# Kernel optimization log

Measured on AMD Instinct MI355X. Metric: run time of the kernel, lower is better.

The kernel has to match this reference:

```python
import jax, jax.numpy as jnp
import numpy as np

B, L, C, W, NH, FS = 8, 8, 64, 32, 128, 5
PAD = FS // 2
LN_EPS = 1e-5


def _conv(x, w, b, pad):
    y = jax.lax.conv_general_dilated(x, w, (1, 1), [(pad, pad), (pad, pad)],
                                     dimension_numbers=('NCHW', 'OIHW', 'NCHW'))
    return y + b[None, :, None, None]


def _stem(x, w1, b1, lnw, lnb, w2, b2):
    # conv(fs) -> LayerNorm over [C,W,W] -> ReLU -> conv(1x1)
    y = _conv(x, w1, b1, PAD)
    mu = jnp.mean(y, axis=(1, 2, 3), keepdims=True)
    var = jnp.var(y, axis=(1, 2, 3), keepdims=True)
    y = (y - mu) * jax.lax.rsqrt(var + LN_EPS) * lnw[None] + lnb[None]
    return _conv(jax.nn.relu(y), w2, b2, 0)


def setup_inputs() -> dict:
    key = jax.random.key(0)
    ks = jax.random.split(key, 8)
    f = lambda k, shp: jax.random.normal(k, shp, jnp.float32) * 0.02
    return {
        'in_query': jax.random.normal(ks[0], (B, C, W, W), jnp.float32),
        'in_keys': jax.random.normal(ks[1], (B, L, C, W, W), jnp.float32),
        'in_values': jax.random.normal(ks[2], (B, L, C, W, W), jnp.float32),
        's_w1': f(ks[3], (C, C, FS, FS)), 's_b1': jnp.zeros((C,), jnp.float32),
        's_lnw': jnp.ones((C, W, W), jnp.float32), 's_lnb': jnp.zeros((C, W, W), jnp.float32),
        's_w2': f(ks[4], (NH, C, 1, 1)), 's_b2': jnp.zeros((NH,), jnp.float32),
        'c_w1': f(ks[5], (C, C, FS, FS)), 'c_b1': jnp.zeros((C,), jnp.float32),
        'c_lnw': jnp.ones((C, W, W), jnp.float32), 'c_lnb': jnp.zeros((C, W, W), jnp.float32),
        'c_w2': f(ks[6], (NH, C, 1, 1)), 'c_b2': jnp.zeros((NH,), jnp.float32),
    }


def reference(in_query, in_keys, in_values,
              s_w1, s_b1, s_lnw, s_lnb, s_w2, s_b2,
              c_w1, c_b1, c_lnw, c_lnb, c_w2, c_b2):
    b, c, w, h = in_query.shape
    l = in_keys.shape[1]
    # ---- spatial attention: tokens = pixels, features = channels ----
    qf = in_query.reshape(b, c, w * h).transpose(0, 2, 1)            # [B, WH, C]
    kf = in_keys.transpose(0, 1, 3, 4, 2).reshape(b, l * w * h, c)   # [B, LWH, C]
    vf = in_values.transpose(0, 1, 3, 4, 2).reshape(b, l * w * h, c)
    a_sp = jax.nn.softmax(jnp.einsum('bnc,bmc->bnm', qf, kf), axis=-1)  # [B, WH, LWH]
    sp = jnp.einsum('bnm,bmc->bnc', a_sp, vf).reshape(b, w, h, c).transpose(0, 3, 1, 2)
    # ---- channel attention: tokens = channels, features = pixels ----
    qc = in_query.reshape(b, c, w * h)                               # [B, C, WH]
    kc = in_keys.reshape(b, l * c, h * w)                            # [B, LC, WH]
    vc = in_values.reshape(b, l * c, h * w)
    a_ch = jax.nn.softmax(jnp.einsum('bcn,bmn->bcm', qc, kc), axis=-1)  # [B, C, LC]
    ch = jnp.einsum('bcm,bmn->bcn', a_ch, vc).reshape(b, c, w, h)
    # ---- conv-LN-ReLU-conv stems on residual-added branches ----
    s_attn = _stem(sp + in_query, s_w1, s_b1, s_lnw, s_lnb, s_w2, s_b2)
    c_attn = _stem(ch + in_query, c_w1, c_b1, c_lnw, c_lnb, c_w2, c_b2)
    return (s_attn, c_attn)
```

## Files before the change

### kernel.cpp

```cpp
#include <hip/hip_runtime.h>


#define LOG2E 1.44269504088896340736f

typedef __attribute__((ext_vector_type(8))) short short8;
typedef __attribute__((ext_vector_type(4))) float f4;

#define MFMA16(a, b, c) __builtin_amdgcn_mfma_f32_16x16x32_bf16(a, b, c, 0, 0, 0)

#define GLOAD_LDS16(gp, lp) __builtin_amdgcn_global_load_lds( \
    (const __attribute__((address_space(1))) void*)(gp), \
    (__attribute__((address_space(3))) void*)(lp), 16, 0, 0)

__device__ __forceinline__ unsigned short f2bf(float f) {
  union { float f; unsigned u; } v; v.f = f;
  unsigned r = v.u + 0x7FFFu + ((v.u >> 16) & 1u);
  return (unsigned short)(r >> 16);
}
__device__ __forceinline__ unsigned short f2bf_rz(float f) {
  union { float f; unsigned u; } v; v.f = f;
  return (unsigned short)(v.u >> 16);
}
__device__ __forceinline__ float bf2f(unsigned short h) {
  union { unsigned u; float f; } v; v.u = ((unsigned)h) << 16;
  return v.f;
}
__device__ __forceinline__ float exp2fast(float x) {
#if __has_builtin(__builtin_amdgcn_exp2f)
  return __builtin_amdgcn_exp2f(x);
#else
  return exp2f(x);
#endif
}

#define O_STATS 0ul
#define O_W1T   256ul
#define O_W2B   409856ul
#define O_LNW   442624ul
#define O_LNB   704768ul
#define O_QT    966912ul
#define O_KSP   2015488ul
#define O_VT    10404096ul
#define O_NUM   18792704ul
#define O_DEN   35569920ul
#define O_SP    36094208ul
#define O_PCH   40288512ul
#define O_XS    40812800ul
#define O_XC    41861376ul
#define O_YT    42909952ul

__global__ __launch_bounds__(256) void k1_prep(
    const float* __restrict__ q, const float* __restrict__ keys,
    const float* __restrict__ values,
    const float* __restrict__ sw1, const float* __restrict__ slnw,
    const float* __restrict__ slnb, const float* __restrict__ sw2,
    const float* __restrict__ cw1, const float* __restrict__ clnw,
    const float* __restrict__ clnb, const float* __restrict__ cw2,
    char* __restrict__ ws)
{
  __shared__ __align__(16) unsigned char SM1[49152];
  const int t = threadIdx.x;

  if (blockIdx.x < 128) {
    float* Sp = (float*)(ws + O_SP);
    const int bid = blockIdx.x;
    if (bid == 0 && t < 64) ((float*)(ws + O_STATS))[t] = 0.f;
    const int b = bid >> 4, colT = (bid >> 2) & 3, kt = bid & 3;
    const int w = t >> 6, lane = t & 63;
    const int low4 = lane & 15, quad = lane >> 4;
    const int dl = lane >> 1, dh = lane & 1;
    const int k00 = kt * 256;

    f4 acc[4][2];
#pragma unroll
    for (int m = 0; m < 4; ++m)
#pragma unroll
      for (int n = 0; n < 2; ++n) acc[m][n] = (f4){0.f, 0.f, 0.f, 0.f};

    auto stageAll = [&](int bo, int k0) {
#pragma unroll
      for (int gi = 0; gi < 4; ++gi) {
        const int g = w + gi * 4;
        const int n = g >> 1, sub = g & 1;
        const int l = sub * 32 + dl;
        const float* gp = keys + (size_t)(b * 512 + colT * 128 + n * 16 + (l & 15)) * 1024
                          + k0 + (l >> 4) * 8 + dh * 4;
        GLOAD_LDS16(gp, SM1 + bo + (size_t)(n * 128 + sub * 64) * 16);
      }
#pragma unroll
      for (int gi = 0; gi < 2; ++gi) {
        const int g = w + gi * 4;
        const int m = g >> 1, sub = g & 1;
        const int l = sub * 32 + dl;
        const float* gp = q + (size_t)(b * 64 + m * 16 + (l & 15)) * 1024
                          + k0 + (l >> 4) * 8 + dh * 4;
        GLOAD_LDS16(gp, SM1 + bo + 16384 + (size_t)(m * 128 + sub * 64) * 16);
      }
    };

    stageAll(0, k00);
    for (int it = 0; it < 8; ++it) {
      const int bo = (it & 1) * 24576;
      const char* cb = (const char*)SM1 + bo;
      __syncthreads();
      if (it < 7) stageAll(bo ^ 24576, k00 + (it + 1) * 32);

      short8 ah[4], al[4];
#pragma unroll
      for (int m = 0; m < 4; ++m) {
        const float* fp = (const float*)(cb + 16384 + (size_t)(m * 128 + lane * 2) * 16);
        float4 u0 = ((const float4*)fp)[0];
        float4 u1 = ((const float4*)fp)[1];
        float vv[8] = {u0.x, u0.y, u0.z, u0.w, u1.x, u1.y, u1.z, u1.w};
#pragma unroll
        for (int j = 0; j < 8; ++j) {
          float sv = vv[j] * LOG2E;
          unsigned short hi = f2bf(sv);
          ah[m][j] = (short)hi;
          al[m][j] = (short)f2bf(sv - bf2f(hi));
        }
      }
#pragma unroll
      for (int n2 = 0; n2 < 2; ++n2) {
        const int n = w * 2 + n2;
        const float* fp = (const float*)(cb + (size_t)(n * 128 + lane * 2) * 16);
        float4 u0 = ((const float4*)fp)[0];
        float4 u1 = ((const float4*)fp)[1];
        float vv[8] = {u0.x, u0.y, u0.z, u0.w, u1.x, u1.y, u1.z, u1.w};
        short8 bh, bl;
#pragma unroll
        for (int j = 0; j < 8; ++j) {
          unsigned short hi = f2bf(vv[j]);
          bh[j] = (short)hi;
          bl[j] = (short)f2bf(vv[j] - bf2f(hi));
        }
#pragma unroll
        for (int m = 0; m < 4; ++m) {
          acc[m][n2] = MFMA16(ah[m], bh, acc[m][n2]);
          acc[m][n2] = MFMA16(al[m], bh, acc[m][n2]);
          acc[m][n2] = MFMA16(ah[m], bl, acc[m][n2]);
        }
      }
    }

#pragma unroll
    for (int m = 0; m < 4; ++m)
#pragma unroll
      for (int n2 = 0; n2 < 2; ++n2)
#pragma unroll
        for (int r = 0; r < 4; ++r) {
          const int row = m * 16 + quad * 4 + r;
          const int col = colT * 128 + (w * 2 + n2) * 16 + low4;
          Sp[(((size_t)kt * 8 + b) * 64 + row) * 512 + col] = acc[m][n2][r];
        }
    return;
  }

  float (*T)[65] = (float(*)[65])SM1;
  const int job = blockIdx.x - 128;

  if (job < 2240) {
    int kind, mat = 0, sel = 0;
    if (job < 1024)      { kind = 0; mat = job >> 4; }
    else if (job < 2048) { kind = 1; mat = (job - 1024) >> 4; }
    else if (job < 2176) { kind = 2; mat = (job - 2048) >> 4; }
    else                 { kind = 3; sel = (job - 2176) >> 4; }
    const int pt = job & 15, p0 = pt * 64;
    const float* src =
        kind == 0 ? keys : kind == 1 ? values : kind == 2 ? q
        : (sel == 0 ? slnw : sel == 1 ? slnb : sel == 2 ? clnw : clnb);
    src += (size_t)mat * 65536;

    const int r0 = t >> 4, c4 = (t & 15) * 4;
    if (kind == 1) {
      unsigned short* VTp = (unsigned short*)(ws + O_VT);
      const int b = mat >> 3, l = mat & 7;
#pragma unroll
      for (int pass = 0; pass < 4; ++pass) {
        const int r = pass * 16 + r0;
        float4 v = *(const float4*)(src + (size_t)r * 1024 + p0 + c4);
        ushort4 o;
        o.x = f2bf(v.x); o.y = f2bf(v.y); o.z = f2bf(v.z); o.w = f2bf(v.w);
        *(ushort4*)(VTp + ((size_t)b * 64 + r) * 8192 + l * 1024 + p0 + c4) = o;
      }
      return;
    }
#pragma unroll
    for (int pass = 0; pass < 4; ++pass) {
      const int r = pass * 16 + r0;
      float4 v = *(const float4*)(src + (size_t)r * 1024 + p0 + c4);
      T[r][c4] = v.x; T[r][c4 + 1] = v.y; T[r][c4 + 2] = v.z; T[r][c4 + 3] = v.w;
    }
    __syncthreads();
#pragma unroll
    for (int pass = 0; pass < 2; ++pass) {
      const int p = pass * 32 + (t >> 3), cs = (t & 7) * 8;
      short8 o;
      if (kind == 0) {
#pragma unroll
        for (int j = 0; j < 8; ++j) o[j] = (short)f2bf(T[cs + j][p] * LOG2E);
        const int b = mat >> 3, l = mat & 7;
        *(short8*)((unsigned short*)(ws + O_KSP) +
                   ((size_t)b * 8192 + l * 1024 + p0 + p) * 64 + cs) = o;
      } else if (kind == 2) {
#pragma unroll
        for (int j = 0; j < 8; ++j) o[j] = (short)f2bf(T[cs + j][p]);
        *(short8*)((unsigned short*)(ws + O_QT) +
                   ((size_t)mat * 1024 + p0 + p) * 64 + cs) = o;
      } else {
#pragma unroll
        for (int j = 0; j < 8; ++j) o[j] = (short)f2bf(T[cs + j][p]);
        unsigned long off = (sel & 1) ? O_LNB : O_LNW;
        *(short8*)((unsigned short*)(ws + off) +
                   ((size_t)(sel >> 1) * 1024 + p0 + p) * 64 + cs) = o;
      }
    }
    return;
  }

  {
    unsigned i = (job - 2240) * 256u + t;
    if (i < 204800u) {
      unsigned ci = i & 63u, co = (i >> 6) & 63u, tt = i >> 12;
      unsigned off = tt % 25u, st = tt / 25u;
      const float* w = st ? cw1 : sw1;
      ((unsigned short*)(ws + O_W1T))[i] = f2bf(w[(co * 64u + ci) * 25u + off]);
      return;
    }
    i -= 204800u;
    if (i < 16384u) {
      unsigned c = i & 63u, nh = (i >> 6) & 127u, st = i >> 13;
      const float* w = st ? cw2 : sw2;
      ((unsigned short*)(ws + O_W2B))[i] = f2bf(w[nh * 64u + c]);
    }
  }
}

__global__ __launch_bounds__(256) void k2_spat(char* __restrict__ ws)
{
  __shared__ __align__(16) unsigned char SM[65536];

  unsigned short (*Kt)[4096] = (unsigned short(*)[4096])(SM);
  unsigned short (*Vt)[4096] = (unsigned short(*)[4096])(SM + 16384);
  unsigned short (*Pl)[4096] = (unsigned short(*)[4096])(SM + 32768);

  const unsigned short* QT = (const unsigned short*)(ws + O_QT);
  const unsigned short* KSP = (const unsigned short*)(ws + O_KSP);
  const unsigned short* VTg = (const unsigned short*)(ws + O_VT);
  unsigned short* NUM = (unsigned short*)(ws + O_NUM);
  float* DEN = (float*)(ws + O_DEN);

  const int b = blockIdx.x >> 6;
  const int qt = (blockIdx.x >> 4) & 3;
  const int s = blockIdx.x & 15;
  const int t = threadIdx.x;
  const int w = t >> 6, lane = t & 63;
  const int low4 = lane & 15, quad = lane >> 4;

  const unsigned short* KSPb = KSP + (size_t)b * 8192 * 64;
  const unsigned short* VTb = VTg + (size_t)b * 64 * 8192;
  const int qbase = qt * 256 + w * 64;
  const int kvbase = s * 512;

  int cn[2], cks[2], cqd[2], cl4[2];
#pragma unroll
  for (int pass = 0; pass < 2; ++pass) {
    const int c = pass * 256 + t;
    cn[pass] = c >> 7; cks[pass] = (c >> 6) & 1;
    cqd[pass] = (c >> 4) & 3; cl4[pass] = c & 15;
  }

  short8 qa[4][2];
#pragma unroll
  for (int mi = 0; mi < 4; ++mi)
#pragma unroll
    for (int ks = 0; ks < 2; ++ks)
      qa[mi][ks] = *(const short8*)(QT +
          ((size_t)(b * 1024 + qbase + mi * 16 + low4)) * 64 + ks * 32 + quad * 8);

  short8 vones;
#pragma unroll
  for (int j = 0; j < 8; ++j) vones[j] = (short)0x3F80;

  f4 accO[4][4], accD[4];
#pragma unroll
  for (int m = 0; m < 4; ++m) {
    accD[m] = (f4){0.f, 0.f, 0.f, 0.f};
#pragma unroll
    for (int n = 0; n < 4; ++n) accO[m][n] = (f4){0.f, 0.f, 0.f, 0.f};
  }

#pragma unroll
  for (int pass = 0; pass < 2; ++pass) {
    GLOAD_LDS16(KSPb + ((size_t)(kvbase + cn[pass] * 16 + cl4[pass])) * 64 +
                    cks[pass] * 32 + cqd[pass] * 8,
                &Kt[0][(pass * 256 + w * 64) * 8]);
    GLOAD_LDS16(VTb + ((size_t)(cn[pass] * 16 + cl4[pass])) * 8192 + kvbase +
                    cks[pass] * 32 + cqd[pass] * 8,
                &Vt[0][(pass * 256 + w * 64) * 8]);
  }

  const int pswz = ((low4 >> 2) & 3) << 1;
  for (int it = 0; it < 8; ++it) {
    const int d = it & 1;
    __syncthreads();
    if (it < 7) {
      const int kv1 = kvbase + (it + 1) * 64;
#pragma unroll
      for (int pass = 0; pass < 2; ++pass) {
        GLOAD_LDS16(KSPb + ((size_t)(kv1 + cn[pass] * 16 + cl4[pass])) * 64 +
                        cks[pass] * 32 + cqd[pass] * 8,
                    &Kt[d ^ 1][(pass * 256 + w * 64) * 8]);
        GLOAD_LDS16(VTb + ((size_t)(cn[pass] * 16 + cl4[pass])) * 8192 + kv1 +
                        cks[pass] * 32 + cqd[pass] * 8,
                    &Vt[d ^ 1][(pass * 256 + w * 64) * 8]);
      }
    }
#pragma unroll
    for (int n = 0; n < 4; ++n) {
      f4 sS[4];
#pragma unroll
      for (int mi = 0; mi < 4; ++mi) sS[mi] = (f4){0.f, 0.f, 0.f, 0.f};
#pragma unroll
      for (int ks = 0; ks < 2; ++ks) {
        short8 kb = *(const short8*)&Kt[d][((n * 2 + ks) * 64 + lane) * 8];
#pragma unroll
        for (int mi = 0; mi < 4; ++mi) sS[mi] = MFMA16(qa[mi][ks], kb, sS[mi]);
      }
      const int cpr = (((n * 2 + (low4 >> 3)) ^ (quad << 1)) << 3) + (low4 & 7);
#pragma unroll
      for (int mi = 0; mi < 4; ++mi) {
        unsigned short* pw = &Pl[w][(mi * 16 + quad * 4) * 64 + cpr];
#pragma unroll
        for (int r = 0; r < 4; ++r)
          pw[r * 64] = f2bf_rz(exp2fast(sS[mi][r]));
      }
    }
#pragma unroll
    for (int ks = 0; ks < 2; ++ks) {
      short8 vb[4];
#pragma unroll
      for (int n2 = 0; n2 < 4; ++n2)
        vb[n2] = *(const short8*)&Vt[d][((n2 * 2 + ks) * 64 + lane) * 8];
      const int cr = (((ks * 4 + quad) ^ pswz) << 3);
#pragma unroll
      for (int m = 0; m < 4; ++m) {
        short8 pa = *(const short8*)&Pl[w][(m * 16 + low4) * 64 + cr];
        accD[m] = MFMA16(pa, vones, accD[m]);
#pragma unroll
        for (int n2 = 0; n2 < 4; ++n2) accO[m][n2] = MFMA16(pa, vb[n2], accO[m][n2]);
      }
    }
  }

#pragma unroll
  for (int m = 0; m < 4; ++m)
#pragma unroll
    for (int r = 0; r < 4; ++r) {
      const int row = qbase + m * 16 + quad * 4 + r;
      const size_t base = ((size_t)(b * 1024 + row) * 16 + s);
#pragma unroll
      for (int n2 = 0; n2 < 4; ++n2)
        NUM[base * 64 + n2 * 16 + low4] = f2bf(accO[m][n2][r]);
      if (low4 == 0) DEN[base] = accD[m][r];
    }
}

__global__ __launch_bounds__(256) void k3_fin_soft(char* __restrict__ ws)
{
  if (blockIdx.x < 512) {
    const unsigned short* NUM = (const unsigned short*)(ws + O_NUM);
    const float* DEN = (const float*)(ws + O_DEN);
    const unsigned short* QT = (const unsigned short*)(ws + O_QT);
    unsigned short* Xs = (unsigned short*)(ws + O_XS);

    const unsigned i = blockIdx.x * 256u + threadIdx.x;
    const int c0 = (i & 15) * 4;
    const unsigned row = i >> 4;

    float dtot = 0.f;
#pragma unroll
    for (int sq = 0; sq < 4; ++sq) {
      float4 dv = *(const float4*)(DEN + (size_t)row * 16 + sq * 4);
      dtot += dv.x + dv.y + dv.z + dv.w;
    }
    float n4[4] = {0.f, 0.f, 0.f, 0.f};
#pragma unroll
    for (int s = 0; s < 16; ++s) {
      ushort4 pv = *(const ushort4*)(NUM + ((size_t)row * 16 + s) * 64 + c0);
      n4[0] += bf2f(pv.x); n4[1] += bf2f(pv.y);
      n4[2] += bf2f(pv.z); n4[3] += bf2f(pv.w);
    }
    const float rd = 1.0f / dtot;
    size_t ob = (size_t)row * 64 + c0;
    ushort4 qv = *(const ushort4*)(QT + ob);
    ushort4 o4;
    o4.x = f2bf(n4[0] * rd + bf2f(qv.x));
    o4.y = f2bf(n4[1] * rd + bf2f(qv.y));
    o4.z = f2bf(n4[2] * rd + bf2f(qv.z));
    o4.w = f2bf(n4[3] * rd + bf2f(qv.w));
    *(ushort4*)(Xs + ob) = o4;
    return;
  }

  {
    const float* Sp = (const float*)(ws + O_SP);
    unsigned short* P = (unsigned short*)(ws + O_PCH);
    const int bid = blockIdx.x - 512;
    const int b = bid >> 2, rt = bid & 3;
    const int row = rt * 16 + (threadIdx.x >> 4), tc = threadIdx.x & 15;

    float sv[32];
    float mx = -1e30f;
#pragma unroll
    for (int jj = 0; jj < 32; ++jj) {
      const int col = jj * 16 + tc;
      size_t base = ((size_t)b * 64 + row) * 512 + col;
      float v = Sp[base] + Sp[base + 262144] + Sp[base + 524288] + Sp[base + 786432];
      sv[jj] = v;
      mx = fmaxf(mx, v);
    }
#pragma unroll
    for (int o = 1; o < 16; o <<= 1) mx = fmaxf(mx, __shfl_xor(mx, o, 64));
    float sum = 0.f;
#pragma unroll
    for (int jj = 0; jj < 32; ++jj) {
      float e = exp2fast(sv[jj] - mx);
      sv[jj] = e;
      sum += e;
    }
#pragma unroll
    for (int o = 1; o < 16; o <<= 1) sum += __shfl_xor(sum, o, 64);
    const float rs = 1.0f / sum;
#pragma unroll
    for (int jj = 0; jj < 32; ++jj)
      P[((size_t)b * 64 + row) * 512 + jj * 16 + tc] = f2bf(sv[jj] * rs);
  }
}

__device__ __forceinline__ void conv5_body(char* ws, const float* b1p, int s, int bid)
{
  __shared__ float Hbuf[2][16][65];
  __shared__ float red[2][2];

  const int b = bid >> 5, pt = bid & 31;
  const int w = threadIdx.x >> 6, lane = threadIdx.x & 63;
  const int low4 = lane & 15, quad = lane >> 4;
  const int wsub = w & 1, half = w >> 1;

  const unsigned short* X = (const unsigned short*)(ws + (s ? O_XC : O_XS));
  const unsigned short* W1t = (const unsigned short*)(ws + O_W1T);
  unsigned short* Yt = (unsigned short*)(ws + O_YT);
  float* stats = (float*)(ws + O_STATS);

  const int p = pt * 32 + wsub * 16 + low4;
  const int y0 = p >> 5, x0 = p & 31;

  f4 acc[4];
#pragma unroll
  for (int m = 0; m < 4; ++m) acc[m] = (f4){0.f, 0.f, 0.f, 0.f};

  const int o0 = half ? 13 : 0, o1 = half ? 25 : 13;
  for (int off = o0; off < o1; ++off) {
    const int dy = off / 5 - 2, dx = off % 5 - 2;
    const int ys = y0 + dy, xs = x0 + dx;
    const bool valid = ((unsigned)ys < 32u) & ((unsigned)xs < 32u);
    const int psrc = valid ? (p + dy * 32 + dx) : p;
    const unsigned short* xp = X + ((size_t)(b * 1024 + psrc)) * 64;
    const unsigned short* wp = W1t + ((size_t)((s * 25 + off) * 64)) * 64;
#pragma unroll
    for (int ks = 0; ks < 2; ++ks) {
      short8 bv = *(const short8*)(xp + ks * 32 + quad * 8);
      if (!valid) bv = (short8)0;
#pragma unroll
      for (int m = 0; m < 4; ++m) {
        short8 av = *(const short8*)(wp + (m * 16 + low4) * 64 + ks * 32 + quad * 8);
        acc[m] = MFMA16(av, bv, acc[m]);
      }
    }
  }

  if (half) {
#pragma unroll
    for (int m = 0; m < 4; ++m)
#pragma unroll
      for (int r = 0; r < 4; ++r)
        Hbuf[wsub][low4][m * 16 + quad * 4 + r] = acc[m][r];
  }
  __syncthreads();
  if (!half) {
    float ls = 0.f, ls2 = 0.f;
#pragma unroll
    for (int m = 0; m < 4; ++m)
#pragma unroll
      for (int r = 0; r < 4; ++r) {
        const int co = m * 16 + quad * 4 + r;
        float y = acc[m][r] + Hbuf[wsub][low4][co] + b1p[co];
        Yt[((size_t)((s * 8 + b) * 1024 + p)) * 64 + co] = f2bf(y);
        ls += y; ls2 += y * y;
      }
#pragma unroll
    for (int o = 1; o < 64; o <<= 1) {
      ls += __shfl_xor(ls, o, 64);
      ls2 += __shfl_xor(ls2, o, 64);
    }
    if (lane == 0) { red[0][wsub] = ls; red[1][wsub] = ls2; }
  }
  __syncthreads();
  if (threadIdx.x == 0) {
    atomicAdd(&stats[(s * 8 + b) * 2 + 0], red[0][0] + red[0][1]);
    atomicAdd(&stats[(s * 8 + b) * 2 + 1], red[1][0] + red[1][1]);
  }
}

__device__ __forceinline__ void final_body(char* ws, const float* b2p,
                                           float* out, int s, int bid)
{
  const int b = bid >> 5, pt = bid & 31;
  const int w = threadIdx.x >> 6, lane = threadIdx.x & 63;
  const int low4 = lane & 15, quad = lane >> 4;
  const int p2 = pt * 32 + (w & 1) * 16 + low4;
  const int nh0 = (w >> 1) * 64;

  const unsigned short* Yt = (const unsigned short*)(ws + O_YT);
  const unsigned short* LNW = (const unsigned short*)(ws + O_LNW);
  const unsigned short* LNB = (const unsigned short*)(ws + O_LNB);
  const unsigned short* W2b = (const unsigned short*)(ws + O_W2B);
  const float* stats = (const float*)(ws + O_STATS);

  const float inv = 1.0f / 65536.0f;
  const float mu = stats[(s * 8 + b) * 2 + 0] * inv;
  const float ms = stats[(s * 8 + b) * 2 + 1] * inv;
  const float rsig = rsqrtf(ms - mu * mu + 1e-5f);

  f4 acc[4];
#pragma unroll
  for (int m = 0; m < 4; ++m) acc[m] = (f4){0.f, 0.f, 0.f, 0.f};

#pragma unroll
  for (int ks = 0; ks < 2; ++ks) {
    size_t yo = ((size_t)((s * 8 + b) * 1024 + p2)) * 64 + ks * 32 + quad * 8;
    size_t lo = ((size_t)(s * 1024 + p2)) * 64 + ks * 32 + quad * 8;
    short8 yv = *(const short8*)(Yt + yo);
    short8 lw8 = *(const short8*)(LNW + lo);
    short8 lb8 = *(const short8*)(LNB + lo);
    short8 zv;
#pragma unroll
    for (int j = 0; j < 8; ++j) {
      float z = (bf2f((unsigned short)yv[j]) - mu) * rsig * bf2f((unsigned short)lw8[j]) +
                bf2f((unsigned short)lb8[j]);
      zv[j] = (short)f2bf(fmaxf(z, 0.f));
    }
#pragma unroll
    for (int m = 0; m < 4; ++m) {
      short8 a = *(const short8*)(W2b + ((size_t)(s * 128 + nh0 + m * 16 + low4)) * 64 + ks * 32 + quad * 8);
      acc[m] = MFMA16(a, zv, acc[m]);
    }
  }
#pragma unroll
  for (int m = 0; m < 4; ++m)
#pragma unroll
    for (int r = 0; r < 4; ++r) {
      const int nh = nh0 + m * 16 + quad * 4 + r;
      out[((size_t)((s * 8 + b) * 128 + nh)) * 1024 + p2] = acc[m][r] + b2p[nh];
    }
}

__global__ __launch_bounds__(256) void k4_conv5s_chanB(
    const float* __restrict__ values, char* __restrict__ ws,
    const float* __restrict__ sb1)
{
  if (blockIdx.x < 256) { conv5_body(ws, sb1, 0, blockIdx.x); return; }

  const unsigned short* P = (const unsigned short*)(ws + O_PCH);
  const unsigned short* QT = (const unsigned short*)(ws + O_QT);
  unsigned short* Xc = (unsigned short*)(ws + O_XC);

  const int bid = blockIdx.x - 256;
  const int b = bid >> 4, pt = bid & 15;
  const int w = threadIdx.x >> 6, lane = threadIdx.x & 63;
  const int low4 = lane & 15, quad = lane >> 4;
  const int p = pt * 64 + w * 16 + low4;

  f4 acc[4];
#pragma unroll
  for (int m = 0; m < 4; ++m) acc[m] = (f4){0.f, 0.f, 0.f, 0.f};

  const float* vbase = values + (size_t)b * 524288 + p;
  for (int ks = 0; ks < 16; ++ks) {
    short8 vbv;
    const float* vp = vbase + (size_t)(ks * 32 + quad * 8) * 1024;
#pragma unroll
    for (int j = 0; j < 8; ++j) vbv[j] = (short)f2bf(vp[(size_t)j * 1024]);
#pragma unroll
    for (int m = 0; m < 4; ++m) {
      short8 a = *(const short8*)(P + ((size_t)(b * 64 + m * 16 + low4)) * 512 + ks * 32 + quad * 8);
      acc[m] = MFMA16(a, vbv, acc[m]);
    }
  }
#pragma unroll
  for (int m = 0; m < 4; ++m)
#pragma unroll
    for (int r = 0; r < 4; ++r) {
      const int c = m * 16 + quad * 4 + r;
      size_t o = ((size_t)(b * 1024 + p)) * 64 + c;
      Xc[o] = f2bf(acc[m][r] + bf2f(QT[o]));
    }
}

__global__ __launch_bounds__(256) void k5_conv5c_finS(
    char* __restrict__ ws, const float* __restrict__ cb1,
    const float* __restrict__ sb2, float* __restrict__ out)
{
  if (blockIdx.x < 256) { conv5_body(ws, cb1, 1, blockIdx.x); return; }
  final_body(ws, sb2, out, 0, blockIdx.x - 256);
}

__global__ __launch_bounds__(256) void k6_finC(
    char* __restrict__ ws, const float* __restrict__ cb2,
    float* __restrict__ out)
{
  final_body(ws, cb2, out, 1, blockIdx.x);
}

extern "C" void kernel_launch(void* const* d_in, const int* in_sizes, int n_in,
                              void* d_out, int out_size, void* d_ws, size_t ws_size,
                              hipStream_t stream)
{
  const float* q    = (const float*)d_in[0];
  const float* keys = (const float*)d_in[1];
  const float* vals = (const float*)d_in[2];
  const float* sw1  = (const float*)d_in[3];
  const float* sb1  = (const float*)d_in[4];
  const float* slnw = (const float*)d_in[5];
  const float* slnb = (const float*)d_in[6];
  const float* sw2  = (const float*)d_in[7];
  const float* sb2  = (const float*)d_in[8];
  const float* cw1  = (const float*)d_in[9];
  const float* cb1  = (const float*)d_in[10];
  const float* clnw = (const float*)d_in[11];
  const float* clnb = (const float*)d_in[12];
  const float* cw2  = (const float*)d_in[13];
  const float* cb2  = (const float*)d_in[14];
  char* ws = (char*)d_ws;

  k1_prep<<<3232, 256, 0, stream>>>(q, keys, vals, sw1, slnw, slnb, sw2,
                                    cw1, clnw, clnb, cw2, ws);
  k2_spat<<<512, 256, 0, stream>>>(ws);
  k3_fin_soft<<<544, 256, 0, stream>>>(ws);
  k4_conv5s_chanB<<<384, 256, 0, stream>>>(vals, ws, sb1);
  k5_conv5c_finS<<<512, 256, 0, stream>>>(ws, cb1, sb2, (float*)d_out);
  k6_finC<<<256, 256, 0, stream>>>(ws, cb2, (float*)d_out);
}
```

Measured before the change: 208.5 us.

## Reschedule stage fusion to merge launches and run both conv stems together

Regroups the six-kernel pipeline into five launches. The channel softmax moves into the spatial attention kernel, the channel P·V product joins the spatial finalize, and both 5x5 conv stems share one launch, as do both final 1x1 stages. This removes one launch boundary and lets independent work fill the grid together. In exchange, the larger fused kernels carry heterogeneous blocks with different resource use, and the 64 KB shared array in k2 now also applies to the softmax blocks.

```diff
diff --git a/kernel.cpp b/kernel.cpp
--- a/kernel.cpp
+++ b/kernel.cpp
@@ -236,9 +236,44 @@
   }
 }
 
-__global__ __launch_bounds__(256) void k2_spat(char* __restrict__ ws)
+__global__ __launch_bounds__(256) void k2_soft_spat(char* __restrict__ ws)
 {
   __shared__ __align__(16) unsigned char SM[65536];
+
+  if (blockIdx.x < 32) {
+    const float* Sp = (const float*)(ws + O_SP);
+    unsigned short* P = (unsigned short*)(ws + O_PCH);
+    const int bid = blockIdx.x;
+    const int b = bid >> 2, rt = bid & 3;
+    const int row = rt * 16 + (threadIdx.x >> 4), tc = threadIdx.x & 15;
+
+    float sv[32];
+    float mx = -1e30f;
+#pragma unroll
+    for (int jj = 0; jj < 32; ++jj) {
+      const int col = jj * 16 + tc;
+      size_t base = ((size_t)b * 64 + row) * 512 + col;
+      float v = Sp[base] + Sp[base + 262144] + Sp[base + 524288] + Sp[base + 786432];
+      sv[jj] = v;
+      mx = fmaxf(mx, v);
+    }
+#pragma unroll
+    for (int o = 1; o < 16; o <<= 1) mx = fmaxf(mx, __shfl_xor(mx, o, 64));
+    float sum = 0.f;
+#pragma unroll
+    for (int jj = 0; jj < 32; ++jj) {
+      float e = exp2fast(sv[jj] - mx);
+      sv[jj] = e;
+      sum += e;
+    }
+#pragma unroll
+    for (int o = 1; o < 16; o <<= 1) sum += __shfl_xor(sum, o, 64);
+    const float rs = 1.0f / sum;
+#pragma unroll
+    for (int jj = 0; jj < 32; ++jj)
+      P[((size_t)b * 64 + row) * 512 + jj * 16 + tc] = f2bf(sv[jj] * rs);
+    return;
+  }
 
   unsigned short (*Kt)[4096] = (unsigned short(*)[4096])(SM);
   unsigned short (*Vt)[4096] = (unsigned short(*)[4096])(SM + 16384);
@@ -250,9 +285,10 @@
   unsigned short* NUM = (unsigned short*)(ws + O_NUM);
   float* DEN = (float*)(ws + O_DEN);
 
-  const int b = blockIdx.x >> 6;
-  const int qt = (blockIdx.x >> 4) & 3;
-  const int s = blockIdx.x & 15;
+  const int bid = blockIdx.x - 32;
+  const int b = bid >> 6;
+  const int qt = (bid >> 4) & 3;
+  const int s = bid & 15;
   const int t = threadIdx.x;
   const int w = t >> 6, lane = t & 63;
   const int low4 = lane & 15, quad = lane >> 4;
@@ -366,15 +402,54 @@
     }
 }
 
-__global__ __launch_bounds__(256) void k3_fin_soft(char* __restrict__ ws)
-{
-  if (blockIdx.x < 512) {
+__global__ __launch_bounds__(256) void k3_chanB_fin(
+    const float* __restrict__ values, char* __restrict__ ws)
+{
+  if (blockIdx.x < 128) {
+    const unsigned short* P = (const unsigned short*)(ws + O_PCH);
+    const unsigned short* QT = (const unsigned short*)(ws + O_QT);
+    unsigned short* Xc = (unsigned short*)(ws + O_XC);
+
+    const int bid = blockIdx.x;
+    const int b = bid >> 4, pt = bid & 15;
+    const int w = threadIdx.x >> 6, lane = threadIdx.x & 63;
+    const int low4 = lane & 15, quad = lane >> 4;
+    const int p = pt * 64 + w * 16 + low4;
+
+    f4 acc[4];
+#pragma unroll
+    for (int m = 0; m < 4; ++m) acc[m] = (f4){0.f, 0.f, 0.f, 0.f};
+
+    const float* vbase = values + (size_t)b * 524288 + p;
+    for (int ks = 0; ks < 16; ++ks) {
+      short8 vbv;
+      const float* vp = vbase + (size_t)(ks * 32 + quad * 8) * 1024;
+#pragma unroll
+      for (int j = 0; j < 8; ++j) vbv[j] = (short)f2bf(vp[(size_t)j * 1024]);
+#pragma unroll
+      for (int m = 0; m < 4; ++m) {
+        short8 a = *(const short8*)(P + ((size_t)(b * 64 + m * 16 + low4)) * 512 + ks * 32 + quad * 8);
+        acc[m] = MFMA16(a, vbv, acc[m]);
+      }
+    }
+#pragma unroll
+    for (int m = 0; m < 4; ++m)
+#pragma unroll
+      for (int r = 0; r < 4; ++r) {
+        const int c = m * 16 + quad * 4 + r;
+        size_t o = ((size_t)(b * 1024 + p)) * 64 + c;
+        Xc[o] = f2bf(acc[m][r] + bf2f(QT[o]));
+      }
+    return;
+  }
+
+  {
     const unsigned short* NUM = (const unsigned short*)(ws + O_NUM);
     const float* DEN = (const float*)(ws + O_DEN);
     const unsigned short* QT = (const unsigned short*)(ws + O_QT);
     unsigned short* Xs = (unsigned short*)(ws + O_XS);
 
-    const unsigned i = blockIdx.x * 256u + threadIdx.x;
+    const unsigned i = (blockIdx.x - 128) * 256u + threadIdx.x;
     const int c0 = (i & 15) * 4;
     const unsigned row = i >> 4;
 
@@ -400,41 +475,6 @@
     o4.z = f2bf(n4[2] * rd + bf2f(qv.z));
     o4.w = f2bf(n4[3] * rd + bf2f(qv.w));
     *(ushort4*)(Xs + ob) = o4;
-    return;
-  }
-
-  {
-    const float* Sp = (const float*)(ws + O_SP);
-    unsigned short* P = (unsigned short*)(ws + O_PCH);
-    const int bid = blockIdx.x - 512;
-    const int b = bid >> 2, rt = bid & 3;
-    const int row = rt * 16 + (threadIdx.x >> 4), tc = threadIdx.x & 15;
-
-    float sv[32];
-    float mx = -1e30f;
-#pragma unroll
-    for (int jj = 0; jj < 32; ++jj) {
-      const int col = jj * 16 + tc;
-      size_t base = ((size_t)b * 64 + row) * 512 + col;
-      float v = Sp[base] + Sp[base + 262144] + Sp[base + 524288] + Sp[base + 786432];
-      sv[jj] = v;
-      mx = fmaxf(mx, v);
-    }
-#pragma unroll
-    for (int o = 1; o < 16; o <<= 1) mx = fmaxf(mx, __shfl_xor(mx, o, 64));
-    float sum = 0.f;
-#pragma unroll
-    for (int jj = 0; jj < 32; ++jj) {
-      float e = exp2fast(sv[jj] - mx);
-      sv[jj] = e;
-      sum += e;
-    }
-#pragma unroll
-    for (int o = 1; o < 16; o <<= 1) sum += __shfl_xor(sum, o, 64);
-    const float rs = 1.0f / sum;
-#pragma unroll
-    for (int jj = 0; jj < 32; ++jj)
-      P[((size_t)b * 64 + row) * 512 + jj * 16 + tc] = f2bf(sv[jj] * rs);
   }
 }
 
@@ -566,61 +606,20 @@
     }
 }
 
-__global__ __launch_bounds__(256) void k4_conv5s_chanB(
-    const float* __restrict__ values, char* __restrict__ ws,
-    const float* __restrict__ sb1)
-{
-  if (blockIdx.x < 256) { conv5_body(ws, sb1, 0, blockIdx.x); return; }
-
-  const unsigned short* P = (const unsigned short*)(ws + O_PCH);
-  const unsigned short* QT = (const unsigned short*)(ws + O_QT);
-  unsigned short* Xc = (unsigned short*)(ws + O_XC);
-
-  const int bid = blockIdx.x - 256;
-  const int b = bid >> 4, pt = bid & 15;
-  const int w = threadIdx.x >> 6, lane = threadIdx.x & 63;
-  const int low4 = lane & 15, quad = lane >> 4;
-  const int p = pt * 64 + w * 16 + low4;
-
-  f4 acc[4];
-#pragma unroll
-  for (int m = 0; m < 4; ++m) acc[m] = (f4){0.f, 0.f, 0.f, 0.f};
-
-  const float* vbase = values + (size_t)b * 524288 + p;
-  for (int ks = 0; ks < 16; ++ks) {
-    short8 vbv;
-    const float* vp = vbase + (size_t)(ks * 32 + quad * 8) * 1024;
-#pragma unroll
-    for (int j = 0; j < 8; ++j) vbv[j] = (short)f2bf(vp[(size_t)j * 1024]);
-#pragma unroll
-    for (int m = 0; m < 4; ++m) {
-      short8 a = *(const short8*)(P + ((size_t)(b * 64 + m * 16 + low4)) * 512 + ks * 32 + quad * 8);
-      acc[m] = MFMA16(a, vbv, acc[m]);
-    }
-  }
-#pragma unroll
-  for (int m = 0; m < 4; ++m)
-#pragma unroll
-    for (int r = 0; r < 4; ++r) {
-      const int c = m * 16 + quad * 4 + r;
-      size_t o = ((size_t)(b * 1024 + p)) * 64 + c;
-      Xc[o] = f2bf(acc[m][r] + bf2f(QT[o]));
-    }
-}
-
-__global__ __launch_bounds__(256) void k5_conv5c_finS(
-    char* __restrict__ ws, const float* __restrict__ cb1,
-    const float* __restrict__ sb2, float* __restrict__ out)
-{
-  if (blockIdx.x < 256) { conv5_body(ws, cb1, 1, blockIdx.x); return; }
-  final_body(ws, sb2, out, 0, blockIdx.x - 256);
-}
-
-__global__ __launch_bounds__(256) void k6_finC(
-    char* __restrict__ ws, const float* __restrict__ cb2,
-    float* __restrict__ out)
-{
-  final_body(ws, cb2, out, 1, blockIdx.x);
+__global__ __launch_bounds__(256) void k4_conv5(
+    char* __restrict__ ws, const float* __restrict__ sb1,
+    const float* __restrict__ cb1)
+{
+  if (blockIdx.x < 256) conv5_body(ws, sb1, 0, blockIdx.x);
+  else                  conv5_body(ws, cb1, 1, blockIdx.x - 256);
+}
+
+__global__ __launch_bounds__(256) void k5_final(
+    char* __restrict__ ws, const float* __restrict__ sb2,
+    const float* __restrict__ cb2, float* __restrict__ out)
+{
+  if (blockIdx.x < 256) final_body(ws, sb2, out, 0, blockIdx.x);
+  else                  final_body(ws, cb2, out, 1, blockIdx.x - 256);
 }
 
 extern "C" void kernel_launch(void* const* d_in, const int* in_sizes, int n_in,
@@ -646,9 +645,8 @@
 
   k1_prep<<<3232, 256, 0, stream>>>(q, keys, vals, sw1, slnw, slnb, sw2,
                                     cw1, clnw, clnb, cw2, ws);
-  k2_spat<<<512, 256, 0, stream>>>(ws);
-  k3_fin_soft<<<544, 256, 0, stream>>>(ws);
-  k4_conv5s_chanB<<<384, 256, 0, stream>>>(vals, ws, sb1);
-  k5_conv5c_finS<<<512, 256, 0, stream>>>(ws, cb1, sb2, (float*)d_out);
-  k6_finC<<<256, 256, 0, stream>>>(ws, cb2, (float*)d_out);
-}
+  k2_soft_spat<<<544, 256, 0, stream>>>(ws);
+  k3_chanB_fin<<<640, 256, 0, stream>>>(vals, ws);
+  k4_conv5<<<512, 256, 0, stream>>>(ws, sb1, cb1);
+  k5_final<<<512, 256, 0, stream>>>(ws, sb2, cb2, (float*)d_out);
+}
```

After: 205.3 us. No clear change (-1.6%).
